# Performance work log

Measured on AMD Instinct MI355X. Metric: run time of the kernel, lower is better.

The kernel has to match this reference:

```python
import jax, jax.numpy as jnp
import numpy as np

B, T, H = 1024, 128, 256
EPS = 1e-5


def _lstm(x, W_ih, W_hh, b_ih, b_hh):
    # x: [B,T,D] -> hs: [B,T,H], hn: [B,H]; PyTorch gate order i,f,g,o
    xp = jnp.einsum('btd,gd->btg', x, W_ih) + b_ih + b_hh  # [B,T,4H]
    h0 = jnp.zeros((x.shape[0], W_hh.shape[1]), x.dtype)

    def step(carry, xt):
        h, c = carry
        g = xt + h @ W_hh.T
        i, f, gg, o = jnp.split(g, 4, axis=-1)
        c = jax.nn.sigmoid(f) * c + jax.nn.sigmoid(i) * jnp.tanh(gg)
        h = jax.nn.sigmoid(o) * jnp.tanh(c)
        return (h, c), h

    (hn, _), hs = jax.lax.scan(step, (h0, h0), jnp.swapaxes(xp, 0, 1))
    return jnp.swapaxes(hs, 0, 1), hn


def _bn(x, g, b, m, v):
    # eval-mode BatchNorm1d
    return g * (x - m) * jax.lax.rsqrt(v + EPS) + b


def setup_inputs() -> dict:
    key = jax.random.key(0)
    ks = jax.random.split(key, 40)
    f = lambda i, shape, s=0.05: jax.random.normal(ks[i], shape, jnp.float32) * s
    d = {}
    d['seq_cont_data'] = f(0, (B, T, 64), 1.0)
    d['seq_cat_data'] = jax.random.randint(ks[1], (B, T, 2), 0, 500)
    d['non_seq_cat_data'] = jax.random.randint(ks[2], (B, 2), 0, 1000)
    d['non_seq_cont_data'] = f(3, (B, 32), 1.0)
    d['emb_ns0'] = f(4, (10000, 64))
    d['emb_ns1'] = f(5, (1000, 64))
    d['emb_s0'] = f(6, (1000, 32))
    d['emb_s1'] = f(7, (500, 32))
    d['W_ih'] = f(8, (4 * H, 128)); d['W_hh'] = f(9, (4 * H, H))
    d['b_ih'] = f(10, (4 * H,)); d['b_hh'] = f(11, (4 * H,))
    d['W_ltd'] = f(12, (H, H)); d['b_ltd'] = f(13, (H,))
    d['W_conv'] = f(14, (H, T)); d['b_conv'] = f(15, (H,))
    d['W_tpa'] = f(16, (H, H)); d['W_tpa_h'] = f(17, (H, H)); d['W_tpa_c'] = f(18, (H, H))
    FIN = 672
    d['W_f1'] = f(19, (512, FIN)); d['b_f1'] = f(20, (512,))
    d['g1'] = 1.0 + f(21, (512,)); d['be1'] = f(22, (512,)); d['m1'] = f(23, (512,)); d['v1'] = jnp.ones((512,), jnp.float32)
    d['W_f2'] = f(24, (256, 512)); d['b_f2'] = f(25, (256,))
    d['g2'] = 1.0 + f(26, (256,)); d['be2'] = f(27, (256,)); d['m2'] = f(28, (256,)); d['v2'] = jnp.ones((256,), jnp.float32)
    d['W_out'] = f(29, (64, 256)); d['b_out'] = f(30, (64,))
    return d


def reference(seq_cont_data, seq_cat_data, non_seq_cat_data, non_seq_cont_data,
              emb_ns0, emb_ns1, emb_s0, emb_s1,
              W_ih, W_hh, b_ih, b_hh, W_ltd, b_ltd, W_conv, b_conv,
              W_tpa, W_tpa_h, W_tpa_c,
              W_f1, b_f1, g1, be1, m1, v1,
              W_f2, b_f2, g2, be2, m2, v2,
              W_out, b_out):
    # non-sequential input: embeddings + continuous
    ns_cat = jnp.concatenate([emb_ns0[non_seq_cat_data[:, 0]], emb_ns1[non_seq_cat_data[:, 1]]], axis=1)
    non_seq_inp = jnp.concatenate([ns_cat, non_seq_cont_data], axis=1)  # [B,160]
    # sequential input: embeddings + continuous
    s_cat = jnp.concatenate([emb_s0[seq_cat_data[:, :, 0]], emb_s1[seq_cat_data[:, :, 1]]], axis=2)
    seq_data = jnp.concatenate([s_cat, seq_cont_data], axis=2)  # [B,T,128]
    output, hn = _lstm(seq_data, W_ih, W_hh, b_ih, b_hh)  # [B,T,H], [B,H]
    # TPA: hc[b,i,j] = Conv1d_j(output[:,:,i]) = sum_t output[b,t,i]*W_conv[j,t] + b_conv[j]
    hc = jnp.einsum('bti,jt->bij', output, W_conv) + b_conv  # [B,H,H]
    # alpha[b,i] = sigmoid( (hc[b,i] @ W_tpa.T) . hn[b] )
    alpha = jax.nn.sigmoid(jnp.einsum('bik,bk->bi', jnp.einsum('bij,kj->bik', hc, W_tpa), hn))
    vt = jnp.einsum('bi,bih->bh', alpha, hc)  # [B,H]
    htprime = hn @ W_tpa_h.T + vt @ W_tpa_c.T
    seq_inp = hn @ W_ltd.T + b_ltd
    fin_input = jnp.concatenate([non_seq_inp, seq_inp, htprime], axis=1)  # [B,672]
    x = _bn(jax.nn.relu(fin_input @ W_f1.T + b_f1), g1, be1, m1, v1)
    x = _bn(jax.nn.relu(x @ W_f2.T + b_f2), g2, be2, m2, v2)
    x = jax.nn.relu(x @ W_out.T + b_out)
    return x, fin_input
```

## Files before the change

kernel.cpp:

```cpp
#include <hip/hip_runtime.h>
#include <hip/hip_bf16.h>
#include <math.h>

#define B_SZ 1024
#define T_SZ 128
#define H_SZ 256
#define DIN  128
#define G4   1024
#define FINW 672

using bf16   = __hip_bfloat16;
using short8 = __attribute__((ext_vector_type(8))) short;
using f32x4  = __attribute__((ext_vector_type(4))) float;

__device__ __forceinline__ float bf2f(bf16 x) { return __bfloat162float(x); }
__device__ __forceinline__ bf16  f2bf(float x) { return __float2bfloat16(x); }
__device__ __forceinline__ float sigm(float x) { return 1.0f / (1.0f + __expf(-x)); }
__device__ __forceinline__ float ftanh(float x) { return 2.0f / (1.0f + __expf(-2.0f * x)) - 1.0f; }

struct Ptrs { const void* p[33]; };

#define NSEG 30
__device__ __host__ constexpr int kSegOffArr(int i) {
  constexpr int off[NSEG + 1] = {
      0,       32768,   672768,  736768,  768768,  784768,  915840,
      1177984, 1179008, 1180032, 1245568, 1245824, 1278592, 1278848,
      1344384, 1409920, 1475456, 1819520, 1820032, 1820544, 1821056,
      1821568, 1822080, 1953152, 1953408, 1953664, 1953920, 1954176,
      1954432, 1970816, 1970880};
  return off[i];
}
#define ARENA_TOTAL 1970880

__global__ __launch_bounds__(256) void k_convert(Ptrs pk, bf16* __restrict__ dst) {
  bool isf32 = ((((const unsigned*)pk.p[24])[0] & 0xFFFFu) == 0u);
  int stride = gridDim.x * blockDim.x;
  for (int i = blockIdx.x * blockDim.x + threadIdx.x; i < ARENA_TOTAL; i += stride) {
    int s = 0, base = 0;
#pragma unroll
    for (int j = 1; j < NSEG; j++) {
      bool ge = (i >= kSegOffArr(j));
      s    = ge ? j : s;
      base = ge ? kSegOffArr(j) : base;
    }
    int off = i - base;
    const void* src = pk.p[3 + s];
    dst[i] = isf32 ? f2bf(((const float*)src)[off]) : ((const bf16*)src)[off];
  }
}

__global__ __launch_bounds__(256) void k_gather(
    const void* __restrict__ seq_cont_raw, const int* __restrict__ seq_cat,
    const bf16* __restrict__ emb_s0, const bf16* __restrict__ emb_s1,
    bf16* __restrict__ seq_out, const unsigned* __restrict__ probe) {
  bool isf32 = ((probe[0] & 0xFFFFu) == 0u);
  int gid = blockIdx.x * blockDim.x + threadIdx.x;
  int seg = gid & 15;
  int m   = gid >> 4;
  int t   = m >> 10;
  int b   = m & 1023;
  bf16* dst = seq_out + (long)m * DIN + seg * 8;
  if (seg < 8) {
    const bf16* src;
    if (seg < 4) {
      int idx = seq_cat[(b * T_SZ + t) * 2 + 0];
      src = emb_s0 + idx * 32 + seg * 8;
    } else {
      int idx = seq_cat[(b * T_SZ + t) * 2 + 1];
      src = emb_s1 + idx * 32 + (seg - 4) * 8;
    }
    *reinterpret_cast<short8*>(dst) = *reinterpret_cast<const short8*>(src);
  } else {
    long base = ((long)b * T_SZ + t) * 64 + (seg - 8) * 8;
    if (isf32) {
      const float4* sp =
          reinterpret_cast<const float4*>((const float*)seq_cont_raw + base);
      float4 x0 = sp[0], x1 = sp[1];
      union { short8 v; bf16 h[8]; } u;
      u.h[0] = f2bf(x0.x); u.h[1] = f2bf(x0.y); u.h[2] = f2bf(x0.z); u.h[3] = f2bf(x0.w);
      u.h[4] = f2bf(x1.x); u.h[5] = f2bf(x1.y); u.h[6] = f2bf(x1.z); u.h[7] = f2bf(x1.w);
      *reinterpret_cast<short8*>(dst) = u.v;
    } else {
      *reinterpret_cast<short8*>(dst) =
          *reinterpret_cast<const short8*>((const bf16*)seq_cont_raw + base);
    }
  }
}

__global__ __launch_bounds__(512, 2) void k_lstm(
    const bf16* __restrict__ seq, const bf16* __restrict__ Wih,
    const bf16* __restrict__ Whh, const bf16* __restrict__ bih,
    const bf16* __restrict__ bhh, bf16* __restrict__ hs) {
  __shared__ short8 hsh[2][8 * 64];
  __shared__ short8 xsh[2][4 * 64];
  int tid  = threadIdx.x;
  int w    = tid >> 6, lane = tid & 63;
  int quad = lane >> 4, l15 = lane & 15;
  int bid  = blockIdx.x;
  int gid  = bid & 63;
  int rank = bid >> 6;
  int peer = 1 - rank;
  int b0   = gid * 16;
  int hup = w * 16 + l15;
  int hu  = rank * 128 + hup;

  { short8 z = {0,0,0,0,0,0,0,0}; hsh[0][tid] = z; }

  float bia[4];
#pragma unroll
  for (int i = 0; i < 4; ++i) {
    int grow = i * H_SZ + hu;
    bia[i] = bf2f(bih[grow]) + bf2f(bhh[grow]);
  }

  short8 wif[4][4];
  short8 whfS[4][4];
  short8 whfP[4][4];
#pragma unroll
  for (int i = 0; i < 4; ++i) {
    long grow = (long)(i * H_SZ + rank * 128 + w * 16 + l15);
#pragma unroll
    for (int kt = 0; kt < 4; ++kt) {
      wif[i][kt] = *reinterpret_cast<const short8*>(
          Wih + grow * DIN + kt * 32 + quad * 8);
      whfS[i][kt] = *reinterpret_cast<const short8*>(
          Whh + grow * H_SZ + (rank * 4 + kt) * 32 + quad * 8);
      whfP[i][kt] = *reinterpret_cast<const short8*>(
          Whh + grow * H_SZ + (peer * 4 + kt) * 32 + quad * 8);
    }
  }
  if (tid < 256)
    xsh[0][tid] = *reinterpret_cast<const short8*>(
        seq + ((long)b0 + (tid & 15)) * DIN + (tid >> 6) * 32 +
        ((tid >> 4) & 3) * 8);
  float c[4] = {0.f, 0.f, 0.f, 0.f};
  __syncthreads();

  for (int t = 0; t < T_SZ; ++t) {
    int cur = t & 1, nxt = cur ^ 1;
    short8 xpre;
    bool dopre = (t + 1 < T_SZ) & (tid < 256);
    if (dopre)
      xpre = *reinterpret_cast<const short8*>(
          seq + ((long)(t + 1) * B_SZ + b0 + (tid & 15)) * DIN +
          (tid >> 6) * 32 + ((tid >> 4) & 3) * 8);

    f32x4 acc[4];
#pragma unroll
    for (int i = 0; i < 4; ++i) acc[i] = {0.f, 0.f, 0.f, 0.f};

#pragma unroll
    for (int kt = 0; kt < 4; ++kt) {
      short8 ax = xsh[cur][kt * 64 + lane];
#pragma unroll
      for (int i = 0; i < 4; ++i)
        acc[i] = __builtin_amdgcn_mfma_f32_16x16x32_bf16(ax, wif[i][kt], acc[i], 0, 0, 0);
    }
#pragma unroll
    for (int kt = 0; kt < 4; ++kt) {
      short8 ah = hsh[cur][(rank * 4 + kt) * 64 + lane];
#pragma unroll
      for (int i = 0; i < 4; ++i)
        acc[i] = __builtin_amdgcn_mfma_f32_16x16x32_bf16(ah, whfS[i][kt], acc[i], 0, 0, 0);
    }

    if (t > 0) {
      if (tid < 256) {
        int m = tid >> 4, seg = tid & 15;
        const unsigned* src = reinterpret_cast<const unsigned*>(
            hs + ((long)(t - 1) * B_SZ + b0 + m) * H_SZ + peer * 128 + seg * 8);
        unsigned d0, d1, d2, d3;
        do {
          d0 = __hip_atomic_load(src + 0, __ATOMIC_RELAXED, __HIP_MEMORY_SCOPE_AGENT);
          d1 = __hip_atomic_load(src + 1, __ATOMIC_RELAXED, __HIP_MEMORY_SCOPE_AGENT);
          d2 = __hip_atomic_load(src + 2, __ATOMIC_RELAXED, __HIP_MEMORY_SCOPE_AGENT);
          d3 = __hip_atomic_load(src + 3, __ATOMIC_RELAXED, __HIP_MEMORY_SCOPE_AGENT);
        } while (d0 == 0xFFFFFFFFu || d1 == 0xFFFFFFFFu ||
                 d2 == 0xFFFFFFFFu || d3 == 0xFFFFFFFFu);
        union { unsigned u[4]; short8 s; } cv;
        cv.u[0] = d0; cv.u[1] = d1; cv.u[2] = d2; cv.u[3] = d3;
        hsh[cur][(peer * 4 + (seg >> 2)) * 64 + (seg & 3) * 16 + m] = cv.s;
      }
      __syncthreads();
    }
#pragma unroll
    for (int kt = 0; kt < 4; ++kt) {
      short8 ah = hsh[cur][(peer * 4 + kt) * 64 + lane];
#pragma unroll
      for (int i = 0; i < 4; ++i)
        acc[i] = __builtin_amdgcn_mfma_f32_16x16x32_bf16(ah, whfP[i][kt], acc[i], 0, 0, 0);
    }

    bf16* hbn = reinterpret_cast<bf16*>(&hsh[nxt][0]);
    unsigned hpk[4];
#pragma unroll
    for (int r = 0; r < 4; ++r) {
      float iv = sigm(acc[0][r] + bia[0]);
      float fv = sigm(acc[1][r] + bia[1]);
      float gv = ftanh(acc[2][r] + bia[2]);
      float ov = sigm(acc[3][r] + bia[3]);
      c[r] = fv * c[r] + iv * gv;
      bf16 hv = f2bf(ov * ftanh(c[r]));
      int m = quad * 4 + r;
      hbn[(((hu >> 5) * 64) + ((hu >> 3) & 3) * 16 + m) * 8 + (hu & 7)] = hv;
      unsigned hraw = (unsigned)*reinterpret_cast<unsigned short*>(&hv);
      unsigned nb = (unsigned)__shfl_down((int)hraw, 1, 64);
      hpk[r] = hraw | (nb << 16);
    }
    if (dopre) xsh[nxt][tid] = xpre;
    __syncthreads();
    if ((l15 & 1) == 0) {
#pragma unroll
      for (int r = 0; r < 4; ++r) {
        int m = quad * 4 + r;
        unsigned* dst = reinterpret_cast<unsigned*>(
            hs + ((long)t * B_SZ + b0 + m) * H_SZ + hu);
        __hip_atomic_store(dst, hpk[r], __ATOMIC_RELAXED,
                           __HIP_MEMORY_SCOPE_AGENT);
      }
    }
  }
}

__global__ __launch_bounds__(256) void k_u(
    const bf16* __restrict__ hs, const bf16* __restrict__ W_tpa,
    const bf16* __restrict__ W_conv, const bf16* __restrict__ b_conv,
    float* __restrict__ w2, float* __restrict__ c0) {
  __shared__ float hn_sh[8][256];
  __shared__ float u_sh[8][256];
  __shared__ float wred[4][8];
  int tid = threadIdx.x;
  long b0 = (long)blockIdx.x * 8;
#pragma unroll
  for (int r = 0; r < 8; r++)
    hn_sh[r][tid] = bf2f(hs[((long)(T_SZ - 1) * B_SZ + b0 + r) * H_SZ + tid]);
  __syncthreads();
  float u[8] = {0,0,0,0,0,0,0,0};
  for (int k = 0; k < H_SZ; k++) {
    float wv = bf2f(W_tpa[k * H_SZ + tid]);
#pragma unroll
    for (int r = 0; r < 8; r++) u[r] += hn_sh[r][k] * wv;
  }
  float bc = bf2f(b_conv[tid]);
  float p[8];
#pragma unroll
  for (int r = 0; r < 8; r++) { u_sh[r][tid] = u[r]; p[r] = u[r] * bc; }
#pragma unroll
  for (int d = 32; d > 0; d >>= 1)
#pragma unroll
    for (int r = 0; r < 8; r++) p[r] += __shfl_down(p[r], d, 64);
  if ((tid & 63) == 0)
#pragma unroll
    for (int r = 0; r < 8; r++) wred[tid >> 6][r] = p[r];
  __syncthreads();
  if (tid < 8)
    c0[b0 + tid] = wred[0][tid] + wred[1][tid] + wred[2][tid] + wred[3][tid];
  if (tid < T_SZ) {
    float a[8] = {0,0,0,0,0,0,0,0};
    for (int j = 0; j < H_SZ; j++) {
      float wv = bf2f(W_conv[j * T_SZ + tid]);
#pragma unroll
      for (int r = 0; r < 8; r++) a[r] += u_sh[r][j] * wv;
    }
#pragma unroll
    for (int r = 0; r < 8; r++) w2[(b0 + r) * T_SZ + tid] = a[r];
  }
}

__global__ __launch_bounds__(256) void k_alphas(
    const bf16* __restrict__ hs, const float* __restrict__ w2,
    const float* __restrict__ c0, float* __restrict__ asum,
    float* __restrict__ sbuf) {
  __shared__ unsigned hc[128 * 129];
  __shared__ float w2s[T_SZ];
  __shared__ float ash[H_SZ];
  __shared__ float red[256];
  int b = blockIdx.x, tid = threadIdx.x;
#pragma unroll
  for (int p = 0; p < 16; p++) {
    int task = p * 256 + tid;
    int row = task >> 5, seg = task & 31;
    short8 v = *reinterpret_cast<const short8*>(
        hs + ((long)row * B_SZ + b) * H_SZ + seg * 8);
    union { short8 s; unsigned u[4]; } cv; cv.s = v;
#pragma unroll
    for (int k = 0; k < 4; k++) hc[row * 129 + seg * 4 + k] = cv.u[k];
  }
  if (tid < T_SZ) w2s[tid] = w2[b * T_SZ + tid];
  __syncthreads();
  {
    float ap = c0[b];
    int wi = tid >> 1, hi = tid & 1;
    for (int t = 0; t < T_SZ; t++) {
      unsigned uv = hc[t * 129 + wi];
      unsigned short h16 = hi ? (unsigned short)(uv >> 16) : (unsigned short)(uv & 0xFFFF);
      float hvf = __bfloat162float(*reinterpret_cast<bf16*>(&h16));
      ap += hvf * w2s[t];
    }
    float a = sigm(ap);
    ash[tid] = a;
    red[tid] = a;
  }
  __syncthreads();
  for (int s = 128; s > 0; s >>= 1) {
    if (tid < s) red[tid] += red[tid + s];
    __syncthreads();
  }
  if (tid == 0) asum[b] = red[0];
  if (tid < T_SZ) {
    float acc = 0.f;
    for (int k = 0; k < 128; k++) {
      int wi = (k + tid) & 127;
      unsigned uv = hc[tid * 129 + wi];
      unsigned short lo16 = (unsigned short)(uv & 0xFFFF);
      unsigned short hi16 = (unsigned short)(uv >> 16);
      float lo = __bfloat162float(*reinterpret_cast<bf16*>(&lo16));
      float hi = __bfloat162float(*reinterpret_cast<bf16*>(&hi16));
      acc += ash[2 * wi] * lo + ash[2 * wi + 1] * hi;
    }
    sbuf[b * T_SZ + tid] = acc;
  }
}

__global__ __launch_bounds__(256) void k_fin(
    const bf16* __restrict__ hs, const float* __restrict__ sbuf,
    const float* __restrict__ asum, const bf16* __restrict__ W_conv,
    const bf16* __restrict__ b_conv, const bf16* __restrict__ W_tpa_h,
    const bf16* __restrict__ W_tpa_c, const bf16* __restrict__ W_ltd,
    const bf16* __restrict__ b_ltd, const int* __restrict__ ns_cat,
    const bf16* __restrict__ emb_ns0, const bf16* __restrict__ emb_ns1,
    const bf16* __restrict__ ns_cont, float* __restrict__ fin,
    void* __restrict__ d_out_raw, const unsigned* __restrict__ probe) {
  bool isf32 = ((probe[0] & 0xFFFFu) == 0u);
  __shared__ float s_sh[8][128];
  __shared__ float hn_sh[8][256];
  __shared__ float vt_sh[8][256];
  int tid = threadIdx.x;
  long b0 = (long)blockIdx.x * 8;
  auto store2 = [&](int r, int pos, float v) {
    fin[(b0 + r) * FINW + pos] = v;
    if (isf32)
      ((float*)d_out_raw + 65536)[(b0 + r) * FINW + pos] = v;
    else
      ((bf16*)d_out_raw + 65536)[(b0 + r) * FINW + pos] = f2bf(v);
  };
  if (tid < 128)
#pragma unroll
    for (int r = 0; r < 8; r++) s_sh[r][tid] = sbuf[(b0 + r) * T_SZ + tid];
#pragma unroll
  for (int r = 0; r < 8; r++)
    hn_sh[r][tid] = bf2f(hs[((long)(T_SZ - 1) * B_SZ + b0 + r) * H_SZ + tid]);
  __syncthreads();
  float vt[8] = {0,0,0,0,0,0,0,0};
  for (int t = 0; t < T_SZ; t++) {
    float wv = bf2f(W_conv[tid * T_SZ + t]);
#pragma unroll
    for (int r = 0; r < 8; r++) vt[r] += wv * s_sh[r][t];
  }
  float bc = bf2f(b_conv[tid]);
#pragma unroll
  for (int r = 0; r < 8; r++) {
    vt[r] += bc * asum[b0 + r];
    vt_sh[r][tid] = vt[r];
  }
  __syncthreads();
  float htp[8] = {0,0,0,0,0,0,0,0}, sq[8] = {0,0,0,0,0,0,0,0};
  for (int k = 0; k < H_SZ; k++) {
    float whk = bf2f(W_tpa_h[tid * H_SZ + k]);
    float wck = bf2f(W_tpa_c[tid * H_SZ + k]);
    float wlk = bf2f(W_ltd[tid * H_SZ + k]);
#pragma unroll
    for (int r = 0; r < 8; r++) {
      htp[r] += hn_sh[r][k] * whk + vt_sh[r][k] * wck;
      sq[r]  += hn_sh[r][k] * wlk;
    }
  }
  float bl = bf2f(b_ltd[tid]);
#pragma unroll
  for (int r = 0; r < 8; r++) {
    store2(r, 160 + tid, sq[r] + bl);
    store2(r, 416 + tid, htp[r]);
  }
  if (tid < 160) {
#pragma unroll
    for (int r = 0; r < 8; r++) {
      long b = b0 + r;
      float v;
      if (tid < 64)       v = bf2f(emb_ns0[(long)ns_cat[b * 2 + 0] * 64 + tid]);
      else if (tid < 128) v = bf2f(emb_ns1[(long)ns_cat[b * 2 + 1] * 64 + tid - 64]);
      else                v = bf2f(ns_cont[b * 32 + tid - 128]);
      store2(r, tid, v);
    }
  }
}

__global__ __launch_bounds__(256) void k_mlp(
    const float* __restrict__ fin, const bf16* __restrict__ W_f1,
    const bf16* __restrict__ b_f1, const bf16* __restrict__ g1,
    const bf16* __restrict__ be1, const bf16* __restrict__ m1,
    const bf16* __restrict__ v1, const bf16* __restrict__ W_f2,
    const bf16* __restrict__ b_f2, const bf16* __restrict__ g2,
    const bf16* __restrict__ be2, const bf16* __restrict__ m2,
    const bf16* __restrict__ v2, const bf16* __restrict__ W_out,
    const bf16* __restrict__ b_out, void* __restrict__ d_out_raw,
    const unsigned* __restrict__ probe) {
  bool isf32 = ((probe[0] & 0xFFFFu) == 0u);
  __shared__ float a_sh[8 * FINW];
  __shared__ float x1_sh[8 * 512];
  __shared__ float x2_sh[8 * 256];
  int tid = threadIdx.x;
  long b0 = (long)blockIdx.x * 8;
  for (int i = tid; i < 8 * FINW; i += 256) a_sh[i] = fin[b0 * FINW + i];
  __syncthreads();
  for (int n = tid; n < 512; n += 256) {
    float acc[8] = {0, 0, 0, 0, 0, 0, 0, 0};
    const bf16* wr = W_f1 + (long)n * FINW;
    for (int k = 0; k < FINW; k++) {
      float wv = bf2f(wr[k]);
#pragma unroll
      for (int r = 0; r < 8; r++) acc[r] += wv * a_sh[r * FINW + k];
    }
    float bb = bf2f(b_f1[n]);
    float scale = bf2f(g1[n]) * rsqrtf(bf2f(v1[n]) + 1e-5f);
    float mm = bf2f(m1[n]), bee = bf2f(be1[n]);
#pragma unroll
    for (int r = 0; r < 8; r++) {
      float x = acc[r] + bb;
      x = x > 0.f ? x : 0.f;
      x1_sh[r * 512 + n] = (x - mm) * scale + bee;
    }
  }
  __syncthreads();
  {
    int n = tid;
    float acc[8] = {0, 0, 0, 0, 0, 0, 0, 0};
    const bf16* wr = W_f2 + (long)n * 512;
    for (int k = 0; k < 512; k++) {
      float wv = bf2f(wr[k]);
#pragma unroll
      for (int r = 0; r < 8; r++) acc[r] += wv * x1_sh[r * 512 + k];
    }
    float bb = bf2f(b_f2[n]);
    float scale = bf2f(g2[n]) * rsqrtf(bf2f(v2[n]) + 1e-5f);
    float mm = bf2f(m2[n]), bee = bf2f(be2[n]);
#pragma unroll
    for (int r = 0; r < 8; r++) {
      float x = acc[r] + bb;
      x = x > 0.f ? x : 0.f;
      x2_sh[r * 256 + n] = (x - mm) * scale + bee;
    }
  }
  __syncthreads();
  if (tid < 64) {
    int n = tid;
    float acc[8] = {0, 0, 0, 0, 0, 0, 0, 0};
    const bf16* wr = W_out + n * H_SZ;
    for (int k = 0; k < H_SZ; k++) {
      float wv = bf2f(wr[k]);
#pragma unroll
      for (int r = 0; r < 8; r++) acc[r] += wv * x2_sh[r * 256 + k];
    }
    float bb = bf2f(b_out[n]);
#pragma unroll
    for (int r = 0; r < 8; r++) {
      float x = acc[r] + bb;
      x = x > 0.f ? x : 0.f;
      if (isf32)
        ((float*)d_out_raw)[(b0 + r) * 64 + n] = x;
      else
        ((bf16*)d_out_raw)[(b0 + r) * 64 + n] = f2bf(x);
    }
  }
}

extern "C" void kernel_launch(void* const* d_in, const int* in_sizes, int n_in,
                              void* d_out, int out_size, void* d_ws,
                              size_t ws_size, hipStream_t stream) {
  const int* seq_cat = (const int*)d_in[1];
  const int* ns_cat  = (const int*)d_in[2];
  const unsigned* probe = (const unsigned*)d_in[24];

  char* ws = (char*)d_ws;
  bf16* seqd  = (bf16*)ws;  ws += (size_t)T_SZ * B_SZ * DIN * 2;
  bf16* hsb   = (bf16*)ws;  ws += (size_t)T_SZ * B_SZ * H_SZ * 2;
  bf16* arena = (bf16*)ws;  ws += (size_t)ARENA_TOTAL * 2;
  float* w2   = (float*)ws; ws += (size_t)B_SZ * T_SZ * 4;
  float* c0   = (float*)ws; ws += (size_t)B_SZ * 4;
  float* asum = (float*)ws; ws += (size_t)B_SZ * 4;
  float* sbuf = (float*)ws; ws += (size_t)B_SZ * T_SZ * 4;
  float* fin  = (float*)ws; ws += (size_t)B_SZ * FINW * 4;

  const bf16* c_ns_cont = arena + 0;
  const bf16* c_emb_ns0 = arena + 32768;
  const bf16* c_emb_ns1 = arena + 672768;
  const bf16* c_emb_s0  = arena + 736768;
  const bf16* c_emb_s1  = arena + 768768;
  const bf16* c_W_ih    = arena + 784768;
  const bf16* c_W_hh    = arena + 915840;
  const bf16* c_b_ih    = arena + 1177984;
  const bf16* c_b_hh    = arena + 1179008;
  const bf16* c_W_ltd   = arena + 1180032;
  const bf16* c_b_ltd   = arena + 1245568;
  const bf16* c_W_conv  = arena + 1245824;
  const bf16* c_b_conv  = arena + 1278592;
  const bf16* c_W_tpa   = arena + 1278848;
  const bf16* c_W_tpa_h = arena + 1344384;
  const bf16* c_W_tpa_c = arena + 1409920;
  const bf16* c_W_f1    = arena + 1475456;
  const bf16* c_b_f1    = arena + 1819520;
  const bf16* c_g1      = arena + 1820032;
  const bf16* c_be1     = arena + 1820544;
  const bf16* c_m1      = arena + 1821056;
  const bf16* c_v1      = arena + 1821568;
  const bf16* c_W_f2    = arena + 1822080;
  const bf16* c_b_f2    = arena + 1953152;
  const bf16* c_g2      = arena + 1953408;
  const bf16* c_be2     = arena + 1953664;
  const bf16* c_m2      = arena + 1953920;
  const bf16* c_v2      = arena + 1954176;
  const bf16* c_W_out   = arena + 1954432;
  const bf16* c_b_out   = arena + 1970816;

  Ptrs pk;
  for (int i = 0; i < 33; i++) pk.p[i] = d_in[i];

  hipMemsetAsync(hsb, 0xFF, (size_t)T_SZ * B_SZ * H_SZ * 2, stream);
  k_convert<<<dim3(512), 256, 0, stream>>>(pk, arena);
  k_gather<<<dim3(B_SZ * T_SZ * 16 / 256), 256, 0, stream>>>(
      d_in[0], seq_cat, c_emb_s0, c_emb_s1, seqd, probe);
  k_lstm<<<dim3(128), 512, 0, stream>>>(seqd, c_W_ih, c_W_hh, c_b_ih, c_b_hh,
                                        hsb);
  k_u<<<dim3(B_SZ / 8), 256, 0, stream>>>(hsb, c_W_tpa, c_W_conv, c_b_conv, w2, c0);
  k_alphas<<<dim3(B_SZ), 256, 0, stream>>>(hsb, w2, c0, asum, sbuf);
  k_fin<<<dim3(B_SZ / 8), 256, 0, stream>>>(hsb, sbuf, asum, c_W_conv, c_b_conv,
                                            c_W_tpa_h, c_W_tpa_c, c_W_ltd,
                                            c_b_ltd, ns_cat, c_emb_ns0,
                                            c_emb_ns1, c_ns_cont, fin, d_out,
                                            probe);
  k_mlp<<<dim3(B_SZ / 8), 256, 0, stream>>>(fin, c_W_f1, c_b_f1, c_g1, c_be1,
                                            c_m1, c_v1, c_W_f2, c_b_f2, c_g2,
                                            c_be2, c_m2, c_v2, c_W_out, c_b_out,
                                            d_out, probe);
}
```

Before: 720.5 us.

## Interleave two batch groups per LSTM block to hide peer hidden-state exchange latency

Each LSTM block now handles two 16-row batch groups (A and B) instead of one, which halves the grid from 128 to 64 blocks. While it waits on the peer block's hidden state for one group, it runs the input and self-recurrent MFMAs of the other. The end-of-step barrier is replaced by an lgkmcnt wait plus a raw s_barrier, and the h stores move into the elementwise loop. This is meant to hide the cross-block polling latency that sits on the serial recurrence path. In exchange, each block does twice as much serial work, and half as many CUs are used.

```diff
diff --git a/kernel.cpp b/kernel.cpp
--- a/kernel.cpp
+++ b/kernel.cpp
@@ -87,24 +87,32 @@
   }
 }
 
+#define HPOISON 0xFFFFFFFFu
 __global__ __launch_bounds__(512, 2) void k_lstm(
     const bf16* __restrict__ seq, const bf16* __restrict__ Wih,
     const bf16* __restrict__ Whh, const bf16* __restrict__ bih,
     const bf16* __restrict__ bhh, bf16* __restrict__ hs) {
-  __shared__ short8 hsh[2][8 * 64];
-  __shared__ short8 xsh[2][4 * 64];
+  __shared__ short8 hshA[2][8 * 64];
+  __shared__ short8 hshB[2][8 * 64];
+  __shared__ short8 xshA[2][4 * 64];
+  __shared__ short8 xshB[2][4 * 64];
   int tid  = threadIdx.x;
   int w    = tid >> 6, lane = tid & 63;
   int quad = lane >> 4, l15 = lane & 15;
   int bid  = blockIdx.x;
-  int gid  = bid & 63;
-  int rank = bid >> 6;
+  int gp   = bid & 31;
+  int rank = bid >> 5;
   int peer = 1 - rank;
-  int b0   = gid * 16;
+  long b0A = (long)gp * 32;
+  long b0B = (long)gp * 32 + 16;
   int hup = w * 16 + l15;
   int hu  = rank * 128 + hup;
 
-  { short8 z = {0,0,0,0,0,0,0,0}; hsh[0][tid] = z; }
+  {
+    short8 z = {0,0,0,0,0,0,0,0};
+    hshA[0][tid] = z;
+    hshB[0][tid] = z;
+  }
 
   float bia[4];
 #pragma unroll
@@ -118,7 +126,7 @@
   short8 whfP[4][4];
 #pragma unroll
   for (int i = 0; i < 4; ++i) {
-    long grow = (long)(i * H_SZ + rank * 128 + w * 16 + l15);
+    long grow = (long)(i * H_SZ + rank * 128 + hup);
 #pragma unroll
     for (int kt = 0; kt < 4; ++kt) {
       wif[i][kt] = *reinterpret_cast<const short8*>(
@@ -129,70 +137,63 @@
           Whh + grow * H_SZ + (peer * 4 + kt) * 32 + quad * 8);
     }
   }
-  if (tid < 256)
-    xsh[0][tid] = *reinterpret_cast<const short8*>(
-        seq + ((long)b0 + (tid & 15)) * DIN + (tid >> 6) * 32 +
-        ((tid >> 4) & 3) * 8);
-  float c[4] = {0.f, 0.f, 0.f, 0.f};
-  __syncthreads();
-
-  for (int t = 0; t < T_SZ; ++t) {
-    int cur = t & 1, nxt = cur ^ 1;
-    short8 xpre;
-    bool dopre = (t + 1 < T_SZ) & (tid < 256);
-    if (dopre)
-      xpre = *reinterpret_cast<const short8*>(
-          seq + ((long)(t + 1) * B_SZ + b0 + (tid & 15)) * DIN +
-          (tid >> 6) * 32 + ((tid >> 4) & 3) * 8);
-
-    f32x4 acc[4];
-#pragma unroll
-    for (int i = 0; i < 4; ++i) acc[i] = {0.f, 0.f, 0.f, 0.f};
-
+  if (tid < 256) {
+    int mm = tid & 15, kt = tid >> 6, qq = (tid >> 4) & 3;
+    xshA[0][tid] = *reinterpret_cast<const short8*>(
+        seq + (b0A + mm) * DIN + kt * 32 + qq * 8);
+    xshB[0][tid] = *reinterpret_cast<const short8*>(
+        seq + (b0B + mm) * DIN + kt * 32 + qq * 8);
+  }
+  float cA[4] = {0.f, 0.f, 0.f, 0.f};
+  float cB[4] = {0.f, 0.f, 0.f, 0.f};
+  short8 xpend;
+  __syncthreads();
+
+  auto mfma_xself = [&](const short8* xbuf, const short8* hbuf, f32x4* acc)
+      __attribute__((always_inline)) {
 #pragma unroll
     for (int kt = 0; kt < 4; ++kt) {
-      short8 ax = xsh[cur][kt * 64 + lane];
+      short8 ax = xbuf[kt * 64 + lane];
 #pragma unroll
       for (int i = 0; i < 4; ++i)
         acc[i] = __builtin_amdgcn_mfma_f32_16x16x32_bf16(ax, wif[i][kt], acc[i], 0, 0, 0);
     }
 #pragma unroll
     for (int kt = 0; kt < 4; ++kt) {
-      short8 ah = hsh[cur][(rank * 4 + kt) * 64 + lane];
+      short8 ah = hbuf[(rank * 4 + kt) * 64 + lane];
 #pragma unroll
       for (int i = 0; i < 4; ++i)
         acc[i] = __builtin_amdgcn_mfma_f32_16x16x32_bf16(ah, whfS[i][kt], acc[i], 0, 0, 0);
     }
-
-    if (t > 0) {
-      if (tid < 256) {
-        int m = tid >> 4, seg = tid & 15;
-        const unsigned* src = reinterpret_cast<const unsigned*>(
-            hs + ((long)(t - 1) * B_SZ + b0 + m) * H_SZ + peer * 128 + seg * 8);
-        unsigned d0, d1, d2, d3;
-        do {
-          d0 = __hip_atomic_load(src + 0, __ATOMIC_RELAXED, __HIP_MEMORY_SCOPE_AGENT);
-          d1 = __hip_atomic_load(src + 1, __ATOMIC_RELAXED, __HIP_MEMORY_SCOPE_AGENT);
-          d2 = __hip_atomic_load(src + 2, __ATOMIC_RELAXED, __HIP_MEMORY_SCOPE_AGENT);
-          d3 = __hip_atomic_load(src + 3, __ATOMIC_RELAXED, __HIP_MEMORY_SCOPE_AGENT);
-        } while (d0 == 0xFFFFFFFFu || d1 == 0xFFFFFFFFu ||
-                 d2 == 0xFFFFFFFFu || d3 == 0xFFFFFFFFu);
-        union { unsigned u[4]; short8 s; } cv;
-        cv.u[0] = d0; cv.u[1] = d1; cv.u[2] = d2; cv.u[3] = d3;
-        hsh[cur][(peer * 4 + (seg >> 2)) * 64 + (seg & 3) * 16 + m] = cv.s;
-      }
-      __syncthreads();
-    }
+  };
+  auto mfma_peer = [&](const short8* hbuf, f32x4* acc)
+      __attribute__((always_inline)) {
 #pragma unroll
     for (int kt = 0; kt < 4; ++kt) {
-      short8 ah = hsh[cur][(peer * 4 + kt) * 64 + lane];
+      short8 ah = hbuf[(peer * 4 + kt) * 64 + lane];
 #pragma unroll
       for (int i = 0; i < 4; ++i)
         acc[i] = __builtin_amdgcn_mfma_f32_16x16x32_bf16(ah, whfP[i][kt], acc[i], 0, 0, 0);
     }
-
-    bf16* hbn = reinterpret_cast<bf16*>(&hsh[nxt][0]);
-    unsigned hpk[4];
+  };
+  auto pollstage = [&](long b0, int tm1, short8* hcur)
+      __attribute__((always_inline)) {
+    int m = tid >> 4, seg = tid & 15;
+    const unsigned* src = reinterpret_cast<const unsigned*>(
+        hs + ((long)tm1 * B_SZ + b0 + m) * H_SZ + peer * 128 + seg * 8);
+    unsigned d0, d1, d2, d3;
+    do {
+      d0 = __hip_atomic_load(src + 0, __ATOMIC_RELAXED, __HIP_MEMORY_SCOPE_AGENT);
+      d1 = __hip_atomic_load(src + 1, __ATOMIC_RELAXED, __HIP_MEMORY_SCOPE_AGENT);
+      d2 = __hip_atomic_load(src + 2, __ATOMIC_RELAXED, __HIP_MEMORY_SCOPE_AGENT);
+      d3 = __hip_atomic_load(src + 3, __ATOMIC_RELAXED, __HIP_MEMORY_SCOPE_AGENT);
+    } while (d0 == HPOISON || d1 == HPOISON || d2 == HPOISON || d3 == HPOISON);
+    union { unsigned u[4]; short8 s; } cv;
+    cv.u[0] = d0; cv.u[1] = d1; cv.u[2] = d2; cv.u[3] = d3;
+    hcur[(peer * 4 + (seg >> 2)) * 64 + (seg & 3) * 16 + m] = cv.s;
+  };
+  auto elemw = [&](f32x4* acc, float (&c)[4], bf16* hbn, long b0, int t)
+      __attribute__((always_inline)) {
 #pragma unroll
     for (int r = 0; r < 4; ++r) {
       float iv = sigm(acc[0][r] + bia[0]);
@@ -205,21 +206,57 @@
       hbn[(((hu >> 5) * 64) + ((hu >> 3) & 3) * 16 + m) * 8 + (hu & 7)] = hv;
       unsigned hraw = (unsigned)*reinterpret_cast<unsigned short*>(&hv);
       unsigned nb = (unsigned)__shfl_down((int)hraw, 1, 64);
-      hpk[r] = hraw | (nb << 16);
-    }
-    if (dopre) xsh[nxt][tid] = xpre;
-    __syncthreads();
-    if ((l15 & 1) == 0) {
-#pragma unroll
-      for (int r = 0; r < 4; ++r) {
-        int m = quad * 4 + r;
+      if ((l15 & 1) == 0) {
         unsigned* dst = reinterpret_cast<unsigned*>(
             hs + ((long)t * B_SZ + b0 + m) * H_SZ + hu);
-        __hip_atomic_store(dst, hpk[r], __ATOMIC_RELAXED,
+        __hip_atomic_store(dst, hraw | (nb << 16), __ATOMIC_RELAXED,
                            __HIP_MEMORY_SCOPE_AGENT);
       }
     }
-  }
+  };
+#define LGKM_BARRIER() do { \
+    asm volatile("s_waitcnt lgkmcnt(0)" ::: "memory"); \
+    __builtin_amdgcn_s_barrier(); } while (0)
+
+  for (int t = 0; t < T_SZ; ++t) {
+    int cur = t & 1, nxt = cur ^ 1;
+    bool ld = (t + 1 < T_SZ) && (tid < 256);
+    short8 xnew;
+
+    if (ld)
+      xnew = *reinterpret_cast<const short8*>(
+          seq + ((long)(t + 1) * B_SZ + b0A + (tid & 15)) * DIN +
+          (tid >> 6) * 32 + ((tid >> 4) & 3) * 8);
+    f32x4 acc[4];
+#pragma unroll
+    for (int i = 0; i < 4; ++i) acc[i] = {0.f, 0.f, 0.f, 0.f};
+    mfma_xself(&xshA[cur][0], &hshA[cur][0], acc);
+    if (tid < 256 && t > 0) {
+      pollstage(b0A, t - 1, &hshA[cur][0]);
+      xshB[cur][tid] = xpend;
+    }
+    LGKM_BARRIER();
+    mfma_peer(&hshA[cur][0], acc);
+    elemw(acc, cA, reinterpret_cast<bf16*>(&hshA[nxt][0]), b0A, t);
+    xpend = xnew;
+
+    if (ld)
+      xnew = *reinterpret_cast<const short8*>(
+          seq + ((long)(t + 1) * B_SZ + b0B + (tid & 15)) * DIN +
+          (tid >> 6) * 32 + ((tid >> 4) & 3) * 8);
+#pragma unroll
+    for (int i = 0; i < 4; ++i) acc[i] = {0.f, 0.f, 0.f, 0.f};
+    mfma_xself(&xshB[cur][0], &hshB[cur][0], acc);
+    if (tid < 256) {
+      if (t > 0) pollstage(b0B, t - 1, &hshB[cur][0]);
+      if (ld) xshA[nxt][tid] = xpend;
+    }
+    LGKM_BARRIER();
+    mfma_peer(&hshB[cur][0], acc);
+    elemw(acc, cB, reinterpret_cast<bf16*>(&hshB[nxt][0]), b0B, t);
+    xpend = xnew;
+  }
+#undef LGKM_BARRIER
 }
 
 __global__ __launch_bounds__(256) void k_u(
@@ -528,8 +565,8 @@
   k_convert<<<dim3(512), 256, 0, stream>>>(pk, arena);
   k_gather<<<dim3(B_SZ * T_SZ * 16 / 256), 256, 0, stream>>>(
       d_in[0], seq_cat, c_emb_s0, c_emb_s1, seqd, probe);
-  k_lstm<<<dim3(128), 512, 0, stream>>>(seqd, c_W_ih, c_W_hh, c_b_ih, c_b_hh,
-                                        hsb);
+  k_lstm<<<dim3(64), 512, 0, stream>>>(seqd, c_W_ih, c_W_hh, c_b_ih, c_b_hh,
+                                       hsb);
   k_u<<<dim3(B_SZ / 8), 256, 0, stream>>>(hsb, c_W_tpa, c_W_conv, c_b_conv, w2, c0);
   k_alphas<<<dim3(B_SZ), 256, 0, stream>>>(hsb, w2, c0, asum, sbuf);
   k_fin<<<dim3(B_SZ / 8), 256, 0, stream>>>(hsb, sbuf, asum, c_W_conv, c_b_conv,
```

New measurement: 1.211 ms. +68.1%, slower.

## Exchange LSTM hidden halves via tagged double-buffered mailbox with fallback polling

Applied to the files above, without the earlier changes.

The LSTM kernel splits each batch group across two cooperating blocks that must swap half of the hidden state every timestep. Instead of polling poisoned entries in the full hs tensor, each block now writes its half into a small double-buffered exchange slot already in MFMA-fragment layout, then publishes a per-step tag. The peer spins on a single tag word before doing one vector load. After a bounded spin it falls back permanently to the old poisoned-value poll. Block-to-group mapping is changed so paired blocks get adjacent IDs, and __syncthreads is replaced with explicit waitcnt plus s_barrier. This adds extra global stores per step and depends on memory ordering between the data stores and the tag store.

```diff
diff --git a/kernel.cpp b/kernel.cpp
--- a/kernel.cpp
+++ b/kernel.cpp
@@ -12,6 +12,7 @@
 using bf16   = __hip_bfloat16;
 using short8 = __attribute__((ext_vector_type(8))) short;
 using f32x4  = __attribute__((ext_vector_type(4))) float;
+using uint4v = __attribute__((ext_vector_type(4))) unsigned;
 
 __device__ __forceinline__ float bf2f(bf16 x) { return __bfloat162float(x); }
 __device__ __forceinline__ bf16  f2bf(float x) { return __float2bfloat16(x); }
@@ -87,20 +88,23 @@
   }
 }
 
+#define HPOISON 0xFFFFFFFFu
+#define FAST_CAP 800
 __global__ __launch_bounds__(512, 2) void k_lstm(
     const bf16* __restrict__ seq, const bf16* __restrict__ Wih,
     const bf16* __restrict__ Whh, const bf16* __restrict__ bih,
-    const bf16* __restrict__ bhh, bf16* __restrict__ hs) {
+    const bf16* __restrict__ bhh, bf16* __restrict__ hs,
+    unsigned* __restrict__ exb, unsigned* __restrict__ tags) {
   __shared__ short8 hsh[2][8 * 64];
   __shared__ short8 xsh[2][4 * 64];
   int tid  = threadIdx.x;
   int w    = tid >> 6, lane = tid & 63;
   int quad = lane >> 4, l15 = lane & 15;
   int bid  = blockIdx.x;
-  int gid  = bid & 63;
-  int rank = bid >> 6;
+  int rank = (bid >> 3) & 1;
   int peer = 1 - rank;
-  int b0   = gid * 16;
+  int gid  = (bid & 7) * 8 + (bid >> 4);
+  long b0  = (long)gid * 16;
   int hup = w * 16 + l15;
   int hu  = rank * 128 + hup;
 
@@ -118,7 +122,7 @@
   short8 whfP[4][4];
 #pragma unroll
   for (int i = 0; i < 4; ++i) {
-    long grow = (long)(i * H_SZ + rank * 128 + w * 16 + l15);
+    long grow = (long)(i * H_SZ + rank * 128 + hup);
 #pragma unroll
     for (int kt = 0; kt < 4; ++kt) {
       wif[i][kt] = *reinterpret_cast<const short8*>(
@@ -131,9 +135,10 @@
   }
   if (tid < 256)
     xsh[0][tid] = *reinterpret_cast<const short8*>(
-        seq + ((long)b0 + (tid & 15)) * DIN + (tid >> 6) * 32 +
+        seq + (b0 + (tid & 15)) * DIN + (tid >> 6) * 32 +
         ((tid >> 4) & 3) * 8);
   float c[4] = {0.f, 0.f, 0.f, 0.f};
+  bool slow = false;
   __syncthreads();
 
   for (int t = 0; t < T_SZ; ++t) {
@@ -164,8 +169,34 @@
         acc[i] = __builtin_amdgcn_mfma_f32_16x16x32_bf16(ah, whfS[i][kt], acc[i], 0, 0, 0);
     }
 
-    if (t > 0) {
-      if (tid < 256) {
+    if (t > 0 && tid < 256) {
+      bool got = false;
+      if (!slow) {
+        const unsigned* tagp =
+            tags + (((gid * 2 + peer) * 2) + ((t - 1) & 1)) * 16;
+        unsigned want = (unsigned)(t - 1), tv;
+        int it = 0;
+        do {
+          asm volatile("global_load_dword %0, %1, off sc0\n\t"
+                       "s_waitcnt vmcnt(0)"
+                       : "=v"(tv) : "v"(tagp) : "memory");
+        } while (tv != want && ++it < FAST_CAP);
+        if (tv == want) {
+          const unsigned* exr =
+              exb + (((gid * 2 + peer) * 2) + ((t - 1) & 1)) * 1024 +
+              (size_t)tid * 4;
+          uint4v dv;
+          asm volatile("global_load_dwordx4 %0, %1, off sc0\n\t"
+                       "s_waitcnt vmcnt(0)"
+                       : "=v"(dv) : "v"(exr) : "memory");
+          union { uint4v u; short8 s; } cv; cv.u = dv;
+          hsh[cur][(peer * 4 + (tid >> 6)) * 64 + (tid & 63)] = cv.s;
+          got = true;
+        } else {
+          slow = true;
+        }
+      }
+      if (!got) {
         int m = tid >> 4, seg = tid & 15;
         const unsigned* src = reinterpret_cast<const unsigned*>(
             hs + ((long)(t - 1) * B_SZ + b0 + m) * H_SZ + peer * 128 + seg * 8);
@@ -175,14 +206,15 @@
           d1 = __hip_atomic_load(src + 1, __ATOMIC_RELAXED, __HIP_MEMORY_SCOPE_AGENT);
           d2 = __hip_atomic_load(src + 2, __ATOMIC_RELAXED, __HIP_MEMORY_SCOPE_AGENT);
           d3 = __hip_atomic_load(src + 3, __ATOMIC_RELAXED, __HIP_MEMORY_SCOPE_AGENT);
-        } while (d0 == 0xFFFFFFFFu || d1 == 0xFFFFFFFFu ||
-                 d2 == 0xFFFFFFFFu || d3 == 0xFFFFFFFFu);
+        } while (d0 == HPOISON || d1 == HPOISON || d2 == HPOISON || d3 == HPOISON);
         union { unsigned u[4]; short8 s; } cv;
         cv.u[0] = d0; cv.u[1] = d1; cv.u[2] = d2; cv.u[3] = d3;
         hsh[cur][(peer * 4 + (seg >> 2)) * 64 + (seg & 3) * 16 + m] = cv.s;
       }
-      __syncthreads();
-    }
+    }
+    asm volatile("s_waitcnt lgkmcnt(0)" ::: "memory");
+    __builtin_amdgcn_s_barrier();
+
 #pragma unroll
     for (int kt = 0; kt < 4; ++kt) {
       short8 ah = hsh[cur][(peer * 4 + kt) * 64 + lane];
@@ -192,6 +224,7 @@
     }
 
     bf16* hbn = reinterpret_cast<bf16*>(&hsh[nxt][0]);
+    unsigned* exd = exb + (((gid * 2 + rank) * 2) + (t & 1)) * 1024;
     unsigned hpk[4];
 #pragma unroll
     for (int r = 0; r < 4; ++r) {
@@ -206,9 +239,23 @@
       unsigned hraw = (unsigned)*reinterpret_cast<unsigned short*>(&hv);
       unsigned nb = (unsigned)__shfl_down((int)hraw, 1, 64);
       hpk[r] = hraw | (nb << 16);
+      if ((l15 & 1) == 0) {
+        int sidx = (hup >> 5) * 512 + ((hup >> 3) & 3) * 128 + m * 8 + (hup & 7);
+        unsigned* dstp = exd + (sidx >> 1);
+        unsigned pkv = hpk[r];
+        asm volatile("global_store_dword %0, %1, off sc0"
+                     :: "v"(dstp), "v"(pkv) : "memory");
+      }
     }
     if (dopre) xsh[nxt][tid] = xpre;
-    __syncthreads();
+    asm volatile("s_waitcnt vmcnt(0) lgkmcnt(0)" ::: "memory");
+    __builtin_amdgcn_s_barrier();
+    if (tid == 0) {
+      unsigned* tagw = tags + (((gid * 2 + rank) * 2) + (t & 1)) * 16;
+      unsigned tv = (unsigned)t;
+      asm volatile("global_store_dword %0, %1, off sc0"
+                   :: "v"(tagw), "v"(tv) : "memory");
+    }
     if ((l15 & 1) == 0) {
 #pragma unroll
       for (int r = 0; r < 4; ++r) {
@@ -489,6 +536,8 @@
   float* asum = (float*)ws; ws += (size_t)B_SZ * 4;
   float* sbuf = (float*)ws; ws += (size_t)B_SZ * T_SZ * 4;
   float* fin  = (float*)ws; ws += (size_t)B_SZ * FINW * 4;
+  unsigned* exb  = (unsigned*)ws; ws += (size_t)64 * 2 * 2 * 1024 * 4;
+  unsigned* tags = (unsigned*)ws; ws += (size_t)64 * 2 * 2 * 16 * 4;
 
   const bf16* c_ns_cont = arena + 0;
   const bf16* c_emb_ns0 = arena + 32768;
@@ -525,11 +574,12 @@
   for (int i = 0; i < 33; i++) pk.p[i] = d_in[i];
 
   hipMemsetAsync(hsb, 0xFF, (size_t)T_SZ * B_SZ * H_SZ * 2, stream);
+  hipMemsetAsync(tags, 0xFF, (size_t)64 * 2 * 2 * 16 * 4, stream);
   k_convert<<<dim3(512), 256, 0, stream>>>(pk, arena);
   k_gather<<<dim3(B_SZ * T_SZ * 16 / 256), 256, 0, stream>>>(
       d_in[0], seq_cat, c_emb_s0, c_emb_s1, seqd, probe);
   k_lstm<<<dim3(128), 512, 0, stream>>>(seqd, c_W_ih, c_W_hh, c_b_ih, c_b_hh,
-                                        hsb);
+                                        hsb, exb, tags);
   k_u<<<dim3(B_SZ / 8), 256, 0, stream>>>(hsb, c_W_tpa, c_W_conv, c_b_conv, w2, c0);
   k_alphas<<<dim3(B_SZ), 256, 0, stream>>>(hsb, w2, c0, asum, sbuf);
   k_fin<<<dim3(B_SZ / 8), 256, 0, stream>>>(hsb, sbuf, asum, c_W_conv, c_b_conv,
```

New measurement: 935.7 us. +29.9%, slower.

## Relax LSTM step barriers and vectorize MLP with transposed activations

Applied to the files above, without the earlier changes.

In the LSTM kernel, __syncthreads is replaced by a barrier that waits only on LDS counters (lgkmcnt), so outstanding global stores no longer stall the barrier. The h stores are also issued directly inside the gate loop, which removes the extra barrier that sat between them. The MLP kernel moves to 512 threads, stores activations transposed so each k reads eight batch rows with float4 loads, and loads weights as vectors. The risk is the memory-ordering assumptions of the custom barrier for the cross-block h exchange.

```diff
diff --git a/kernel.cpp b/kernel.cpp
--- a/kernel.cpp
+++ b/kernel.cpp
@@ -10,6 +10,7 @@
 #define FINW 672
 
 using bf16   = __hip_bfloat16;
+using short4v = __attribute__((ext_vector_type(4))) short;
 using short8 = __attribute__((ext_vector_type(8))) short;
 using f32x4  = __attribute__((ext_vector_type(4))) float;
 
@@ -17,6 +18,10 @@
 __device__ __forceinline__ bf16  f2bf(float x) { return __float2bfloat16(x); }
 __device__ __forceinline__ float sigm(float x) { return 1.0f / (1.0f + __expf(-x)); }
 __device__ __forceinline__ float ftanh(float x) { return 2.0f / (1.0f + __expf(-2.0f * x)) - 1.0f; }
+__device__ __forceinline__ float bfraw2f(unsigned short r) {
+  unsigned u = ((unsigned)r) << 16;
+  return *reinterpret_cast<float*>(&u);
+}
 
 struct Ptrs { const void* p[33]; };
 
@@ -87,6 +92,7 @@
   }
 }
 
+#define HPOISON 0xFFFFFFFFu
 __global__ __launch_bounds__(512, 2) void k_lstm(
     const bf16* __restrict__ seq, const bf16* __restrict__ Wih,
     const bf16* __restrict__ Whh, const bf16* __restrict__ bih,
@@ -100,7 +106,7 @@
   int gid  = bid & 63;
   int rank = bid >> 6;
   int peer = 1 - rank;
-  int b0   = gid * 16;
+  long b0  = (long)gid * 16;
   int hup = w * 16 + l15;
   int hu  = rank * 128 + hup;
 
@@ -118,7 +124,7 @@
   short8 whfP[4][4];
 #pragma unroll
   for (int i = 0; i < 4; ++i) {
-    long grow = (long)(i * H_SZ + rank * 128 + w * 16 + l15);
+    long grow = (long)(i * H_SZ + rank * 128 + hup);
 #pragma unroll
     for (int kt = 0; kt < 4; ++kt) {
       wif[i][kt] = *reinterpret_cast<const short8*>(
@@ -131,10 +137,14 @@
   }
   if (tid < 256)
     xsh[0][tid] = *reinterpret_cast<const short8*>(
-        seq + ((long)b0 + (tid & 15)) * DIN + (tid >> 6) * 32 +
+        seq + (b0 + (tid & 15)) * DIN + (tid >> 6) * 32 +
         ((tid >> 4) & 3) * 8);
   float c[4] = {0.f, 0.f, 0.f, 0.f};
   __syncthreads();
+
+#define LGKM_BARRIER() do { \
+    asm volatile("s_waitcnt lgkmcnt(0)" ::: "memory"); \
+    __builtin_amdgcn_s_barrier(); } while (0)
 
   for (int t = 0; t < T_SZ; ++t) {
     int cur = t & 1, nxt = cur ^ 1;
@@ -175,13 +185,12 @@
           d1 = __hip_atomic_load(src + 1, __ATOMIC_RELAXED, __HIP_MEMORY_SCOPE_AGENT);
           d2 = __hip_atomic_load(src + 2, __ATOMIC_RELAXED, __HIP_MEMORY_SCOPE_AGENT);
           d3 = __hip_atomic_load(src + 3, __ATOMIC_RELAXED, __HIP_MEMORY_SCOPE_AGENT);
-        } while (d0 == 0xFFFFFFFFu || d1 == 0xFFFFFFFFu ||
-                 d2 == 0xFFFFFFFFu || d3 == 0xFFFFFFFFu);
+        } while (d0 == HPOISON || d1 == HPOISON || d2 == HPOISON || d3 == HPOISON);
         union { unsigned u[4]; short8 s; } cv;
         cv.u[0] = d0; cv.u[1] = d1; cv.u[2] = d2; cv.u[3] = d3;
         hsh[cur][(peer * 4 + (seg >> 2)) * 64 + (seg & 3) * 16 + m] = cv.s;
       }
-      __syncthreads();
+      LGKM_BARRIER();
     }
 #pragma unroll
     for (int kt = 0; kt < 4; ++kt) {
@@ -192,7 +201,6 @@
     }
 
     bf16* hbn = reinterpret_cast<bf16*>(&hsh[nxt][0]);
-    unsigned hpk[4];
 #pragma unroll
     for (int r = 0; r < 4; ++r) {
       float iv = sigm(acc[0][r] + bia[0]);
@@ -205,21 +213,17 @@
       hbn[(((hu >> 5) * 64) + ((hu >> 3) & 3) * 16 + m) * 8 + (hu & 7)] = hv;
       unsigned hraw = (unsigned)*reinterpret_cast<unsigned short*>(&hv);
       unsigned nb = (unsigned)__shfl_down((int)hraw, 1, 64);
-      hpk[r] = hraw | (nb << 16);
-    }
-    if (dopre) xsh[nxt][tid] = xpre;
-    __syncthreads();
-    if ((l15 & 1) == 0) {
-#pragma unroll
-      for (int r = 0; r < 4; ++r) {
-        int m = quad * 4 + r;
+      if ((l15 & 1) == 0) {
         unsigned* dst = reinterpret_cast<unsigned*>(
             hs + ((long)t * B_SZ + b0 + m) * H_SZ + hu);
-        __hip_atomic_store(dst, hpk[r], __ATOMIC_RELAXED,
+        __hip_atomic_store(dst, hraw | (nb << 16), __ATOMIC_RELAXED,
                            __HIP_MEMORY_SCOPE_AGENT);
       }
     }
-  }
+    if (dopre) xsh[nxt][tid] = xpre;
+    LGKM_BARRIER();
+  }
+#undef LGKM_BARRIER
 }
 
 __global__ __launch_bounds__(256) void k_u(
@@ -394,7 +398,7 @@
   }
 }
 
-__global__ __launch_bounds__(256) void k_mlp(
+__global__ __launch_bounds__(512) void k_mlp(
     const float* __restrict__ fin, const bf16* __restrict__ W_f1,
     const bf16* __restrict__ b_f1, const bf16* __restrict__ g1,
     const bf16* __restrict__ be1, const bf16* __restrict__ m1,
@@ -405,20 +409,32 @@
     const bf16* __restrict__ b_out, void* __restrict__ d_out_raw,
     const unsigned* __restrict__ probe) {
   bool isf32 = ((probe[0] & 0xFFFFu) == 0u);
-  __shared__ float a_sh[8 * FINW];
-  __shared__ float x1_sh[8 * 512];
-  __shared__ float x2_sh[8 * 256];
+  __shared__ float a_sh[FINW * 8];
+  __shared__ float x1t[512 * 8];
+  __shared__ float x2t[256 * 8];
   int tid = threadIdx.x;
   long b0 = (long)blockIdx.x * 8;
-  for (int i = tid; i < 8 * FINW; i += 256) a_sh[i] = fin[b0 * FINW + i];
-  __syncthreads();
-  for (int n = tid; n < 512; n += 256) {
+  for (int i = tid; i < 8 * FINW; i += 512) {
+    int r = i / FINW, k = i - r * FINW;
+    a_sh[k * 8 + r] = fin[b0 * FINW + i];
+  }
+  __syncthreads();
+  {
+    int n = tid;
     float acc[8] = {0, 0, 0, 0, 0, 0, 0, 0};
-    const bf16* wr = W_f1 + (long)n * FINW;
-    for (int k = 0; k < FINW; k++) {
-      float wv = bf2f(wr[k]);
-#pragma unroll
-      for (int r = 0; r < 8; r++) acc[r] += wv * a_sh[r * FINW + k];
+    const short4v* wr4 = reinterpret_cast<const short4v*>(W_f1 + (long)n * FINW);
+    for (int kk = 0; kk < FINW / 4; kk++) {
+      short4v w4 = wr4[kk];
+#pragma unroll
+      for (int j = 0; j < 4; j++) {
+        float wv = bfraw2f((unsigned short)w4[j]);
+        const float4* ap = reinterpret_cast<const float4*>(&a_sh[(kk * 4 + j) * 8]);
+        float4 a0 = ap[0], a1 = ap[1];
+        acc[0] += wv * a0.x; acc[1] += wv * a0.y;
+        acc[2] += wv * a0.z; acc[3] += wv * a0.w;
+        acc[4] += wv * a1.x; acc[5] += wv * a1.y;
+        acc[6] += wv * a1.z; acc[7] += wv * a1.w;
+      }
     }
     float bb = bf2f(b_f1[n]);
     float scale = bf2f(g1[n]) * rsqrtf(bf2f(v1[n]) + 1e-5f);
@@ -427,18 +443,26 @@
     for (int r = 0; r < 8; r++) {
       float x = acc[r] + bb;
       x = x > 0.f ? x : 0.f;
-      x1_sh[r * 512 + n] = (x - mm) * scale + bee;
-    }
-  }
-  __syncthreads();
-  {
+      x1t[n * 8 + r] = (x - mm) * scale + bee;
+    }
+  }
+  __syncthreads();
+  if (tid < 256) {
     int n = tid;
     float acc[8] = {0, 0, 0, 0, 0, 0, 0, 0};
-    const bf16* wr = W_f2 + (long)n * 512;
-    for (int k = 0; k < 512; k++) {
-      float wv = bf2f(wr[k]);
-#pragma unroll
-      for (int r = 0; r < 8; r++) acc[r] += wv * x1_sh[r * 512 + k];
+    const short8* wr8 = reinterpret_cast<const short8*>(W_f2 + (long)n * 512);
+    for (int kk = 0; kk < 64; kk++) {
+      short8 w8 = wr8[kk];
+#pragma unroll
+      for (int j = 0; j < 8; j++) {
+        float wv = bfraw2f((unsigned short)w8[j]);
+        const float4* ap = reinterpret_cast<const float4*>(&x1t[(kk * 8 + j) * 8]);
+        float4 a0 = ap[0], a1 = ap[1];
+        acc[0] += wv * a0.x; acc[1] += wv * a0.y;
+        acc[2] += wv * a0.z; acc[3] += wv * a0.w;
+        acc[4] += wv * a1.x; acc[5] += wv * a1.y;
+        acc[6] += wv * a1.z; acc[7] += wv * a1.w;
+      }
     }
     float bb = bf2f(b_f2[n]);
     float scale = bf2f(g2[n]) * rsqrtf(bf2f(v2[n]) + 1e-5f);
@@ -447,18 +471,26 @@
     for (int r = 0; r < 8; r++) {
       float x = acc[r] + bb;
       x = x > 0.f ? x : 0.f;
-      x2_sh[r * 256 + n] = (x - mm) * scale + bee;
+      x2t[n * 8 + r] = (x - mm) * scale + bee;
     }
   }
   __syncthreads();
   if (tid < 64) {
     int n = tid;
     float acc[8] = {0, 0, 0, 0, 0, 0, 0, 0};
-    const bf16* wr = W_out + n * H_SZ;
-    for (int k = 0; k < H_SZ; k++) {
-      float wv = bf2f(wr[k]);
-#pragma unroll
-      for (int r = 0; r < 8; r++) acc[r] += wv * x2_sh[r * 256 + k];
+    const short8* wr8 = reinterpret_cast<const short8*>(W_out + (long)n * H_SZ);
+    for (int kk = 0; kk < 32; kk++) {
+      short8 w8 = wr8[kk];
+#pragma unroll
+      for (int j = 0; j < 8; j++) {
+        float wv = bfraw2f((unsigned short)w8[j]);
+        const float4* ap = reinterpret_cast<const float4*>(&x2t[(kk * 8 + j) * 8]);
+        float4 a0 = ap[0], a1 = ap[1];
+        acc[0] += wv * a0.x; acc[1] += wv * a0.y;
+        acc[2] += wv * a0.z; acc[3] += wv * a0.w;
+        acc[4] += wv * a1.x; acc[5] += wv * a1.y;
+        acc[6] += wv * a1.z; acc[7] += wv * a1.w;
+      }
     }
     float bb = bf2f(b_out[n]);
 #pragma unroll
@@ -537,7 +569,7 @@
                                             c_b_ltd, ns_cat, c_emb_ns0,
                                             c_emb_ns1, c_ns_cont, fin, d_out,
                                             probe);
-  k_mlp<<<dim3(B_SZ / 8), 256, 0, stream>>>(fin, c_W_f1, c_b_f1, c_g1, c_be1,
+  k_mlp<<<dim3(B_SZ / 8), 512, 0, stream>>>(fin, c_W_f1, c_b_f1, c_g1, c_be1,
                                             c_m1, c_v1, c_W_f2, c_b_f2, c_g2,
                                             c_be2, c_m2, c_v2, c_W_out, c_b_out,
                                             d_out, probe);
```

New measurement: 716.5 us. No clear change (-0.6%).
